# Optimization experiments

Measured on AMD Instinct MI355X. Metric: run time of the kernel, lower is better.

## Reference

```python
import jax, jax.numpy as jnp
import numpy as np

STATE_DIM = 1024
INPUT_DIM = 1024
OUTPUT_DIM = 1024
BATCH = 8
SEQ = 2048


def setup_inputs() -> dict:
    key = jax.random.key(0)
    k_x, k_a, k_b, k_w, k_bias = jax.random.split(key, 5)
    x = jax.random.normal(k_x, (BATCH, SEQ, INPUT_DIM), dtype=jnp.float32)
    # diagonal transition a in (0, 0.99) for stability
    A = jax.random.uniform(k_a, (STATE_DIM,), dtype=jnp.float32, minval=0.0, maxval=0.99)
    B = jax.random.normal(k_b, (STATE_DIM, INPUT_DIM), dtype=jnp.float32) / np.sqrt(INPUT_DIM)
    W = jax.random.normal(k_w, (OUTPUT_DIM, STATE_DIM), dtype=jnp.float32) / np.sqrt(STATE_DIM)
    b = jax.random.normal(k_bias, (OUTPUT_DIM,), dtype=jnp.float32) * 0.01
    return {"x": x, "A": A, "B": B, "W": W, "b": b}


def reference(x, A, B, W, b):
    # x: [batch, seq, input_dim]
    # Input projection: u_t = B x_t  -> [batch, seq, state_dim]
    u = jnp.einsum('bld,nd->bln', x, B)
    # Diagonal linear recurrence h_t = A * h_{t-1} + u_t via associative scan.
    # Pair representation (a, b) composes as (a1*a2, a2*b1 + b2).
    aa = jnp.broadcast_to(A, u.shape)

    def combine(c1, c2):
        a1, b1 = c1
        a2, b2 = c2
        return a1 * a2, a2 * b1 + b2

    _, h = jax.lax.associative_scan(combine, (aa, u), axis=1)
    # Output projection: [batch, seq, output_dim]
    return jnp.einsum('bln,on->blo', h, W) + b
```

## Files before the change

### kernel.cpp

```cpp
#include <hip/hip_runtime.h>
#include <stdint.h>

#define BATCH 8
#define SEQ 2048
#define DIM 1024
#define MTOT (BATCH * SEQ)

typedef __attribute__((ext_vector_type(8))) short short8;
typedef __attribute__((ext_vector_type(8))) unsigned short ushort8;
typedef __attribute__((ext_vector_type(4))) float floatx4;


__device__ __forceinline__ unsigned short f2bf(float f) {
  union { float f; unsigned u; } c; c.f = f;
  unsigned u = c.u;
  return (unsigned short)((u + 0x7FFFu + ((u >> 16) & 1u)) >> 16);
}
__device__ __forceinline__ float bf2f(unsigned short h) {
  union { unsigned u; float f; } c; c.u = ((unsigned)h) << 16;
  return c.f;
}

__device__ __forceinline__ void gll16(const void* g, void* l) {
  __builtin_amdgcn_global_load_lds(
      (__attribute__((address_space(1))) void*)(uintptr_t)g,
      (__attribute__((address_space(3))) void*)(uintptr_t)l,
      16, 0, 0);
}


#define X4 (MTOT * DIM / 4)
#define M4 (DIM * DIM / 4)

__global__ __launch_bounds__(256) void cast3_kernel(
    const float* __restrict__ x, const float* __restrict__ B,
    const float* __restrict__ W, unsigned short* __restrict__ xb,
    unsigned short* __restrict__ Bb, unsigned short* __restrict__ Wb) {
  int i = blockIdx.x * 256 + threadIdx.x;
  const float4* s4;
  uint2* d2;
  int li;
  if (i < X4) {
    s4 = (const float4*)x; d2 = (uint2*)xb; li = i;
  } else if (i < X4 + M4) {
    s4 = (const float4*)B; d2 = (uint2*)Bb; li = i - X4;
  } else {
    s4 = (const float4*)W; d2 = (uint2*)Wb; li = i - X4 - M4;
  }
  float4 v = s4[li];
  uint2 o;
  o.x = (unsigned)f2bf(v.x) | ((unsigned)f2bf(v.y) << 16);
  o.y = (unsigned)f2bf(v.z) | ((unsigned)f2bf(v.w) << 16);
  d2[li] = o;
}


__global__ __launch_bounds__(256) void gemm1_r3(
    const unsigned short* __restrict__ A,
    const unsigned short* __restrict__ B,
    unsigned short* __restrict__ u,
    const float* __restrict__ Adiag,
    float* __restrict__ aggbuf) {
  __shared__ unsigned short smem[24576];
  __shared__ float segsum[2][128];

  const int tid = threadIdx.x;
  const int wave = tid >> 6, lane = tid & 63;

  const int id = blockIdx.x;
  const int xcd = id & 7, j = id >> 3;
  const int mt = xcd * 16 + (j >> 3);
  const int nt = j & 7;
  const size_t m0 = (size_t)mt * 128;
  const int n0 = nt * 128;

  floatx4 acc[4][4] = {};

  const int srow0 = wave * 16 + ((tid & 63) >> 2);
  const int colg = (tid & 3) ^ ((tid >> 2) & 3);
  const unsigned short* gA = A + (m0 + srow0) * 1024 + colg * 8;
  const unsigned short* gB = B + ((size_t)n0 + srow0) * 1024 + colg * 8;
  const int wofs = wave * 512;

  const int fr = lane & 15;
  const int fm3 = fr & 3;
  const int kb = lane >> 4;
  const int wm = (wave & 1) * 64, wn = (wave >> 1) * 64;

#define STG(tt, s)                                                          \
  {                                                                         \
    const int kt_ = (tt) * 32;                                              \
    unsigned short* a_ = smem + (s) * 4096 + wofs;                          \
    unsigned short* b_ = smem + 12288 + (s) * 4096 + wofs;                  \
    gll16(gA + kt_, a_);                                                    \
    gll16(gA + (size_t)64 * 1024 + kt_, a_ + 2048);                         \
    gll16(gB + kt_, b_);                                                    \
    gll16(gB + (size_t)64 * 1024 + kt_, b_ + 2048);                         \
  }

  STG(0, 0);
  STG(1, 1);
  asm volatile("s_waitcnt vmcnt(4)" ::: "memory");
  __syncthreads();

  for (int t = 0; t < 32; ++t) {
    if (t + 2 < 32) STG(t + 2, (t + 2) % 3);

    const unsigned short* sA = smem + (t % 3) * 4096;
    const unsigned short* sB = smem + 12288 + (t % 3) * 4096;
    short8 af[4], bfv[4];
#pragma unroll
    for (int i = 0; i < 4; ++i)
      af[i] = *(const short8*)(sA + (wm + i * 16 + fr) * 32 +
                               ((kb ^ fm3) * 8));
#pragma unroll
    for (int jj = 0; jj < 4; ++jj)
      bfv[jj] = *(const short8*)(sB + (wn + jj * 16 + fr) * 32 +
                                 ((kb ^ fm3) * 8));
    __builtin_amdgcn_s_setprio(1);
#pragma unroll
    for (int i = 0; i < 4; ++i)
#pragma unroll
      for (int jj = 0; jj < 4; ++jj)
        acc[i][jj] = __builtin_amdgcn_mfma_f32_16x16x32_bf16(
            af[i], bfv[jj], acc[i][jj], 0, 0, 0);
    __builtin_amdgcn_s_setprio(0);

    if (t + 2 < 32)
      asm volatile("s_waitcnt vmcnt(4)" ::: "memory");
    else
      asm volatile("s_waitcnt vmcnt(0)" ::: "memory");
    __syncthreads();
  }
#undef STG

  const int col = lane & 15;
  const int row4 = (lane >> 4) * 4;
  unsigned short* sC = smem;
#pragma unroll
  for (int i = 0; i < 4; ++i)
#pragma unroll
    for (int jj = 0; jj < 4; ++jj)
#pragma unroll
      for (int r = 0; r < 4; ++r)
        sC[(wm + i * 16 + row4 + r) * 128 + wn + jj * 16 + col] =
            f2bf(acc[i][jj][r]);
  __syncthreads();

  const int colv = tid & 127;
  const int seg = tid >> 7;
  const float a = Adiag[n0 + colv];
  {
    float s = 0.f;
    const int t0 = seg * 64;
#pragma unroll 8
    for (int t = 0; t < 64; ++t) {
      int idx = (t0 + t) * 128 + colv;
      s = fmaf(a, s, bf2f(sC[idx]));
      sC[idx] = f2bf(s);
    }
    segsum[seg][colv] = s;
  }
  __syncthreads();

  {
    float a2 = a * a, a4 = a2 * a2, a8 = a4 * a4, a16 = a8 * a8;
    float a32 = a16 * a16, a64 = a32 * a32;
    const float s0 = segsum[0][colv];
    const int t0 = 64 + seg * 32;
    float apow = seg ? a32 * a : a;
#pragma unroll 8
    for (int t = 0; t < 32; ++t) {
      int idx = (t0 + t) * 128 + colv;
      sC[idx] = f2bf(fmaf(apow, s0, bf2f(sC[idx])));
      apow *= a;
    }
    if (seg)
      aggbuf[(size_t)mt * 1024 + n0 + colv] =
          fmaf(a64, s0, segsum[1][colv]);
  }
  __syncthreads();

#pragma unroll
  for (int s = 0; s < 8; ++s) {
    int row = wave * 32 + s * 4 + (lane >> 4);
    int c8 = (lane & 15) * 8;
    *(ushort8*)(u + (m0 + row) * (size_t)1024 + n0 + c8) =
        *(const ushort8*)(sC + row * 128 + c8);
  }
}


__global__ __launch_bounds__(256) void apply_combined(
    unsigned short* __restrict__ u, const float* __restrict__ Adiag,
    const float* __restrict__ agg) {
  const int id = blockIdx.x;
  const int xcd = id & 7, rem = id >> 3;
  const int mt = xcd * 16 + (rem >> 4);
  if ((mt & 15) == 0) return;
  const int sub = rem & 15;
  const int tg = threadIdx.x >> 7;
  const int ch0 = (threadIdx.x & 127) * 8;

  float a[8];
  *(float4*)&a[0] = *(const float4*)(Adiag + ch0);
  *(float4*)&a[4] = *(const float4*)(Adiag + ch0 + 4);

  float cf[8];
  {
    const int b = mt >> 4, c = mt & 15;
    float aL[8];
#pragma unroll
    for (int jj = 0; jj < 8; ++jj) aL[jj] = a[jj];
#pragma unroll
    for (int i = 0; i < 7; ++i)
#pragma unroll
      for (int jj = 0; jj < 8; ++jj) aL[jj] *= aL[jj];
#pragma unroll
    for (int jj = 0; jj < 8; ++jj) cf[jj] = 0.f;
    for (int cp = 0; cp < c; ++cp) {
      const float* ap = agg + (size_t)(b * 16 + cp) * 1024 + ch0;
      float lv[8];
      *(float4*)&lv[0] = *(const float4*)ap;
      *(float4*)&lv[4] = *(const float4*)(ap + 4);
#pragma unroll
      for (int jj = 0; jj < 8; ++jj) cf[jj] = fmaf(aL[jj], cf[jj], lv[jj]);
    }
  }

  const int tl = sub * 8 + tg * 4;
  float apow[8];
#pragma unroll
  for (int j = 0; j < 8; ++j)
    apow[j] = __builtin_amdgcn_exp2f(__builtin_amdgcn_logf(a[j]) *
                                     (float)(tl + 1));
  const size_t base = ((size_t)mt * 128 + tl) * DIM + ch0;
#pragma unroll
  for (int s = 0; s < 4; ++s) {
    ushort8 v = *(const ushort8*)(u + base + (size_t)s * DIM);
    ushort8 o;
#pragma unroll
    for (int j = 0; j < 8; ++j) {
      o[j] = f2bf(fmaf(apow[j], cf[j], bf2f(v[j])));
      apow[j] *= a[j];
    }
    *(ushort8*)(u + base + (size_t)s * DIM) = o;
  }
}


__global__ __launch_bounds__(512, 2) void gemm2_pipe(
    const unsigned short* __restrict__ A,
    const unsigned short* __restrict__ Bw,
    float* __restrict__ C, const float* __restrict__ bias) {
  extern __shared__ unsigned short sm[];

  const int tid = threadIdx.x;
  const int wid = tid >> 6, lane = tid & 63;

  const int id = blockIdx.x;
  const int xcd = id & 7, j = id >> 3;
  const int mt = xcd * 8 + (j >> 3);
  const int nt = j & 7;
  const size_t m0 = (size_t)mt * 256;
  const int n0 = nt * 128;

  floatx4 acc[4][4] = {};

  const int srow = tid >> 3;
  const int scolg = (tid & 7) ^ (srow & 7);
  const unsigned short* gA = A + (m0 + srow) * 1024 + scolg * 8;
  const unsigned short* gB = Bw + ((size_t)n0 + srow) * 1024 + scolg * 8;

  const int fr = lane & 15;
  const int frs = fr & 7;
  const int kb = lane >> 4;
  const int wm = (wid >> 1) * 64;
  const int wn = (wid & 1) * 64;

#define G2_STAGE(tt, s)                                                     \
  {                                                                         \
    const int kt_ = (tt) * 64;                                              \
    unsigned short* a_ = sm + (s) * 16384 + wid * 512;                      \
    unsigned short* b_ = sm + 49152 + (s) * 8192 + wid * 512;               \
    _Pragma("unroll") for (int r = 0; r < 4; ++r)                           \
        gll16(gA + (size_t)r * 64 * 1024 + kt_, a_ + r * 4096);             \
    _Pragma("unroll") for (int r = 0; r < 2; ++r)                           \
        gll16(gB + (size_t)r * 64 * 1024 + kt_, b_ + r * 4096);             \
  }

  G2_STAGE(0, 0);
  G2_STAGE(1, 1);
  asm volatile("s_waitcnt vmcnt(6)" ::: "memory");
  __syncthreads();

  for (int t = 0; t < 16; ++t) {
    if (t + 2 < 16) G2_STAGE(t + 2, (t + 2) % 3);

    const unsigned short* sA = sm + (t % 3) * 16384;
    const unsigned short* sB = sm + 49152 + (t % 3) * 8192;
    short8 af[4][2], bfv[4][2];
#pragma unroll
    for (int kk = 0; kk < 2; ++kk) {
#pragma unroll
      for (int i = 0; i < 4; ++i)
        af[i][kk] = *(const short8*)(sA + (wm + i * 16 + fr) * 64 +
                                     (((kk * 4 + kb) ^ frs) * 8));
#pragma unroll
      for (int jj = 0; jj < 4; ++jj)
        bfv[jj][kk] = *(const short8*)(sB + (wn + jj * 16 + fr) * 64 +
                                       (((kk * 4 + kb) ^ frs) * 8));
    }
    __builtin_amdgcn_s_setprio(1);
#pragma unroll
    for (int kk = 0; kk < 2; ++kk)
#pragma unroll
      for (int i = 0; i < 4; ++i)
#pragma unroll
        for (int jj = 0; jj < 4; ++jj)
          acc[i][jj] = __builtin_amdgcn_mfma_f32_16x16x32_bf16(
              af[i][kk], bfv[jj][kk], acc[i][jj], 0, 0, 0);
    __builtin_amdgcn_s_setprio(0);

    if (t + 2 < 16)
      asm volatile("s_waitcnt vmcnt(6)" ::: "memory");
    else
      asm volatile("s_waitcnt vmcnt(0)" ::: "memory");
    __syncthreads();
  }
#undef G2_STAGE

  const int col = lane & 15;
  const int row4 = (lane >> 4) * 4;
#pragma unroll
  for (int i = 0; i < 4; ++i)
#pragma unroll
    for (int jj = 0; jj < 4; ++jj)
#pragma unroll
      for (int r = 0; r < 4; ++r) {
        size_t m = m0 + wm + i * 16 + row4 + r;
        int n = n0 + wn + jj * 16 + col;
        C[m * 1024 + n] = acc[i][jj][r] + bias[n];
      }
}


extern "C" void kernel_launch(void* const* d_in, const int* in_sizes, int n_in,
                              void* d_out, int out_size, void* d_ws,
                              size_t ws_size, hipStream_t stream) {
  const float* x    = (const float*)d_in[0];
  const float* A    = (const float*)d_in[1];
  const float* B    = (const float*)d_in[2];
  const float* W    = (const float*)d_in[3];
  const float* bias = (const float*)d_in[4];

  char* ws = (char*)d_ws;
  unsigned short* xb   = (unsigned short*)ws;
  unsigned short* ubuf = (unsigned short*)(ws + 33554432);
  unsigned short* Bb   = (unsigned short*)(ws + 67108864);
  unsigned short* Wb   = (unsigned short*)(ws + 69206016);
  float* aggbuf        = (float*)(ws + 71303168);

  static bool attr_set = false;
  if (!attr_set) {
    hipFuncSetAttribute(reinterpret_cast<const void*>(gemm2_pipe),
                        hipFuncAttributeMaxDynamicSharedMemorySize, 147456);
    attr_set = true;
  }

  cast3_kernel<<<(X4 + 2 * M4) / 256, 256, 0, stream>>>(x, B, W, xb, Bb, Wb);

  gemm1_r3<<<1024, 256, 0, stream>>>(xb, Bb, ubuf, A, aggbuf);

  apply_combined<<<2048, 256, 0, stream>>>(ubuf, A, aggbuf);

  gemm2_pipe<<<512, 512, 147456, stream>>>(ubuf, Wb, (float*)d_out, bias);
}
```

Baseline: 228.8 us.

## Fuse fp32-to-bf16 conversion of x into the first GEMM's LDS loads

Result: slower. 242.4 us (+5.9%).

```diff
diff --git a/kernel.cpp b/kernel.cpp
--- a/kernel.cpp
+++ b/kernel.cpp
@@ -1,4 +1,5 @@
 #include <hip/hip_runtime.h>
+#include <hip/hip_bf16.h>
 #include <stdint.h>
 
 #define BATCH 8
@@ -19,6 +20,11 @@
 __device__ __forceinline__ float bf2f(unsigned short h) {
   union { unsigned u; float f; } c; c.u = ((unsigned)h) << 16;
   return c.f;
+}
+__device__ __forceinline__ unsigned short cvtbf(float f) {
+  __hip_bfloat16 h = __float2bfloat16(f);
+  union { __hip_bfloat16 h; unsigned short u; } c; c.h = h;
+  return c.u;
 }
 
 __device__ __forceinline__ void gll16(const void* g, void* l) {
@@ -29,23 +35,19 @@
 }
 
 
-#define X4 (MTOT * DIM / 4)
 #define M4 (DIM * DIM / 4)
 
-__global__ __launch_bounds__(256) void cast3_kernel(
-    const float* __restrict__ x, const float* __restrict__ B,
-    const float* __restrict__ W, unsigned short* __restrict__ xb,
+__global__ __launch_bounds__(256) void cast2_kernel(
+    const float* __restrict__ B, const float* __restrict__ W,
     unsigned short* __restrict__ Bb, unsigned short* __restrict__ Wb) {
   int i = blockIdx.x * 256 + threadIdx.x;
   const float4* s4;
   uint2* d2;
   int li;
-  if (i < X4) {
-    s4 = (const float4*)x; d2 = (uint2*)xb; li = i;
-  } else if (i < X4 + M4) {
-    s4 = (const float4*)B; d2 = (uint2*)Bb; li = i - X4;
+  if (i < M4) {
+    s4 = (const float4*)B; d2 = (uint2*)Bb; li = i;
   } else {
-    s4 = (const float4*)W; d2 = (uint2*)Wb; li = i - X4 - M4;
+    s4 = (const float4*)W; d2 = (uint2*)Wb; li = i - M4;
   }
   float4 v = s4[li];
   uint2 o;
@@ -55,13 +57,13 @@
 }
 
 
-__global__ __launch_bounds__(256) void gemm1_r3(
-    const unsigned short* __restrict__ A,
+__global__ __launch_bounds__(256) void gemm1_x32(
+    const float* __restrict__ X,
     const unsigned short* __restrict__ B,
     unsigned short* __restrict__ u,
     const float* __restrict__ Adiag,
     float* __restrict__ aggbuf) {
-  __shared__ unsigned short smem[24576];
+  __shared__ unsigned short smem[36864];
   __shared__ float segsum[2][128];
 
   const int tid = threadIdx.x;
@@ -76,43 +78,54 @@
 
   floatx4 acc[4][4] = {};
 
+  const int arow = wave * 8 + (lane >> 3);
+  const int ag = (lane & 7) ^ ((lane >> 3) & 7);
+  const float* gX = X + (m0 + arow) * 1024 + ag * 4;
   const int srow0 = wave * 16 + ((tid & 63) >> 2);
   const int colg = (tid & 3) ^ ((tid >> 2) & 3);
-  const unsigned short* gA = A + (m0 + srow0) * 1024 + colg * 8;
   const unsigned short* gB = B + ((size_t)n0 + srow0) * 1024 + colg * 8;
   const int wofs = wave * 512;
 
   const int fr = lane & 15;
   const int fm3 = fr & 3;
+  const int fm7 = fr & 7;
   const int kb = lane >> 4;
   const int wm = (wave & 1) * 64, wn = (wave >> 1) * 64;
 
 #define STG(tt, s)                                                          \
   {                                                                         \
     const int kt_ = (tt) * 32;                                              \
-    unsigned short* a_ = smem + (s) * 4096 + wofs;                          \
-    unsigned short* b_ = smem + 12288 + (s) * 4096 + wofs;                  \
-    gll16(gA + kt_, a_);                                                    \
-    gll16(gA + (size_t)64 * 1024 + kt_, a_ + 2048);                         \
+    unsigned short* a_ = smem + (s) * 8192 + wave * 512;                    \
+    unsigned short* b_ = smem + 24576 + (s) * 4096 + wofs;                  \
+    _Pragma("unroll") for (int r = 0; r < 4; ++r)                           \
+        gll16(gX + (size_t)r * 32 * 1024 + kt_, a_ + r * 2048);             \
     gll16(gB + kt_, b_);                                                    \
     gll16(gB + (size_t)64 * 1024 + kt_, b_ + 2048);                         \
   }
 
   STG(0, 0);
   STG(1, 1);
-  asm volatile("s_waitcnt vmcnt(4)" ::: "memory");
+  asm volatile("s_waitcnt vmcnt(6)" ::: "memory");
   __syncthreads();
 
   for (int t = 0; t < 32; ++t) {
     if (t + 2 < 32) STG(t + 2, (t + 2) % 3);
 
-    const unsigned short* sA = smem + (t % 3) * 4096;
-    const unsigned short* sB = smem + 12288 + (t % 3) * 4096;
+    const float* sA = (const float*)(smem) + (t % 3) * 4096;
+    const unsigned short* sB = smem + 24576 + (t % 3) * 4096;
     short8 af[4], bfv[4];
 #pragma unroll
-    for (int i = 0; i < 4; ++i)
-      af[i] = *(const short8*)(sA + (wm + i * 16 + fr) * 32 +
-                               ((kb ^ fm3) * 8));
+    for (int i = 0; i < 4; ++i) {
+      const int row = wm + i * 16 + fr;
+      float4 lo = *(const float4*)(sA + row * 32 + (((2 * kb) ^ fm7) * 4));
+      float4 hi = *(const float4*)(sA + row * 32 + (((2 * kb + 1) ^ fm7) * 4));
+      ushort8 o;
+      o[0] = cvtbf(lo.x); o[1] = cvtbf(lo.y);
+      o[2] = cvtbf(lo.z); o[3] = cvtbf(lo.w);
+      o[4] = cvtbf(hi.x); o[5] = cvtbf(hi.y);
+      o[6] = cvtbf(hi.z); o[7] = cvtbf(hi.w);
+      af[i] = *(short8*)&o;
+    }
 #pragma unroll
     for (int jj = 0; jj < 4; ++jj)
       bfv[jj] = *(const short8*)(sB + (wn + jj * 16 + fr) * 32 +
@@ -127,7 +140,7 @@
     __builtin_amdgcn_s_setprio(0);
 
     if (t + 2 < 32)
-      asm volatile("s_waitcnt vmcnt(4)" ::: "memory");
+      asm volatile("s_waitcnt vmcnt(6)" ::: "memory");
     else
       asm volatile("s_waitcnt vmcnt(0)" ::: "memory");
     __syncthreads();
@@ -355,11 +368,10 @@
   const float* bias = (const float*)d_in[4];
 
   char* ws = (char*)d_ws;
-  unsigned short* xb   = (unsigned short*)ws;
-  unsigned short* ubuf = (unsigned short*)(ws + 33554432);
-  unsigned short* Bb   = (unsigned short*)(ws + 67108864);
-  unsigned short* Wb   = (unsigned short*)(ws + 69206016);
-  float* aggbuf        = (float*)(ws + 71303168);
+  unsigned short* ubuf = (unsigned short*)ws;
+  unsigned short* Bb   = (unsigned short*)(ws + 33554432);
+  unsigned short* Wb   = (unsigned short*)(ws + 35651584);
+  float* aggbuf        = (float*)(ws + 37748736);
 
   static bool attr_set = false;
   if (!attr_set) {
@@ -368,9 +380,9 @@
     attr_set = true;
   }
 
-  cast3_kernel<<<(X4 + 2 * M4) / 256, 256, 0, stream>>>(x, B, W, xb, Bb, Wb);
-
-  gemm1_r3<<<1024, 256, 0, stream>>>(xb, Bb, ubuf, A, aggbuf);
+  cast2_kernel<<<2 * M4 / 256, 256, 0, stream>>>(B, W, Bb, Wb);
+
+  gemm1_x32<<<1024, 256, 0, stream>>>(x, Bb, ubuf, A, aggbuf);
 
   apply_combined<<<2048, 256, 0, stream>>>(ubuf, A, aggbuf);
 
```
